# Kernel tuning notes

Hardware: AMD Instinct MI355X
Metric: run time of the kernel (lower is better)

## Reference

```python
import jax, jax.numpy as jnp
import numpy as np

D_MODEL = 512
N_HEAD = 8
D_HEAD = D_MODEL // N_HEAD


def _linear(x, W, b):
    return x @ W + b


def setup_inputs() -> dict:
    key = jax.random.key(0)
    ks = jax.random.split(key, 20)
    B, N, D = 8, 1024, D_MODEL
    H = D // 2
    s = 1.0 / np.sqrt(D)
    s2 = 1.0 / np.sqrt(H)
    inp = {
        'query': jax.random.normal(ks[0], (B, N, D), jnp.float32),
        'key_in': jax.random.normal(ks[1], (B, N, D), jnp.float32),
        'value': jax.random.normal(ks[2], (B, N, D), jnp.float32),
        'Wq': jax.random.normal(ks[3], (D, D), jnp.float32) * s,
        'bq': jnp.zeros((D,), jnp.float32),
        'Wk': jax.random.normal(ks[4], (D, D), jnp.float32) * s,
        'bk': jnp.zeros((D,), jnp.float32),
        'Wv': jax.random.normal(ks[5], (D, D), jnp.float32) * s,
        'bv': jnp.zeros((D,), jnp.float32),
        'Wo': jax.random.normal(ks[6], (D, D), jnp.float32) * s,
        'bo': jnp.zeros((D,), jnp.float32),
        'Ws1': jax.random.normal(ks[7], (D, H), jnp.float32) * s,
        'bs1': jnp.zeros((H,), jnp.float32),
        'Ws2': jax.random.normal(ks[8], (H, D), jnp.float32) * s2,
        'bs2': jnp.zeros((D,), jnp.float32),
        'Wc1': jax.random.normal(ks[9], (D, H), jnp.float32) * s,
        'bc1': jnp.zeros((H,), jnp.float32),
        'Wc2': jax.random.normal(ks[10], (H, D), jnp.float32) * s2,
        'bc2': jnp.zeros((D,), jnp.float32),
    }
    return inp


def reference(query, key_in, value, Wq, bq, Wk, bk, Wv, bv, Wo, bo,
              Ws1, bs1, Ws2, bs2, Wc1, bc1, Wc2, bc2):
    B, N, D = query.shape
    H, Dh = N_HEAD, D_HEAD

    def split_heads(x):  # [b, n, h*d] -> [b, h, n, d]
        return x.reshape(B, N, H, Dh).transpose(0, 2, 1, 3)

    q = split_heads(_linear(query, Wq, bq))
    k = split_heads(_linear(key_in, Wk, bk))
    vv = _linear(value, Wv, bv)  # [b, n, d] == rearrange(v,'b h n d->b n (h d)')

    # spatial gating: Linear-ReLU-Linear-Sigmoid on w_v(value)
    sw = jax.nn.sigmoid(_linear(jax.nn.relu(_linear(vv, Ws1, bs1)), Ws2, bs2))
    v_spatial = split_heads(vv * sw)

    # channel gating: MLP on mean-over-seq profile, broadcast back to seq
    prof = value.mean(axis=1, keepdims=True)  # [b, 1, d]
    cw = jax.nn.sigmoid(_linear(jax.nn.relu(_linear(prof, Wc1, bc1)), Wc2, bc2))
    v_channel = split_heads(_linear(value * cw, Wv, bv))

    v_dual = v_spatial + v_channel

    scores = jnp.einsum('bhqd,bhkd->bhqk', q, k) / np.sqrt(Dh).astype(np.float32)
    attn = jax.nn.softmax(scores, axis=-1)
    out = jnp.einsum('bhqk,bhkd->bhqd', attn, v_dual)
    out = out.transpose(0, 2, 1, 3).reshape(B, N, D)
    return _linear(out, Wo, bo)  # dropout is identity in eval mode
```

## Files before the change

### kernel.cpp

```cpp
#include <hip/hip_runtime.h>

typedef unsigned short u16t;
typedef __bf16  bf8   __attribute__((ext_vector_type(8)));
typedef float   f32x4 __attribute__((ext_vector_type(4)));
typedef unsigned short us4 __attribute__((ext_vector_type(4)));

#define DEV __device__ __forceinline__

DEV float bf2f(u16t u) { union { unsigned u; float f; } x; x.u = ((unsigned)u) << 16; return x.f; }
DEV u16t  f2bf(float f) {
    union { float f; unsigned u; } x; x.f = f;
    unsigned r = x.u + 0x7FFFu + ((x.u >> 16) & 1u);
    return (u16t)(r >> 16);
}
DEV uint4 pack8(const float* v) {
    uint4 r;
    r.x = (unsigned)f2bf(v[0]) | ((unsigned)f2bf(v[1]) << 16);
    r.y = (unsigned)f2bf(v[2]) | ((unsigned)f2bf(v[3]) << 16);
    r.z = (unsigned)f2bf(v[4]) | ((unsigned)f2bf(v[5]) << 16);
    r.w = (unsigned)f2bf(v[6]) | ((unsigned)f2bf(v[7]) << 16);
    return r;
}
DEV void gll16(const void* g, void* l) {
    __builtin_amdgcn_global_load_lds(
        (const __attribute__((address_space(1))) unsigned*)g,
        (__attribute__((address_space(3))) unsigned*)l, 16, 0, 0);
}

#define DMODEL 512
#define SEQ    1024
#define NBATCH 8

__global__ __launch_bounds__(256) void fill_sentinel(float* out, int n)
{
    int i = blockIdx.x * 256 + threadIdx.x;
    if (i < n) out[i] = 100.f;
}

__global__ __launch_bounds__(256) void cvt_value(const float* v, u16t* Vi)
{
    size_t i = ((size_t)blockIdx.x * 256 + threadIdx.x) * 8;
    float4 a = *(const float4*)(v + i), b = *(const float4*)(v + i + 4);
    float o[8] = {a.x, a.y, a.z, a.w, b.x, b.y, b.z, b.w};
    *(uint4*)&Vi[i] = pack8(o);
}

__global__ __launch_bounds__(256) void transpose6(
    const float* s0, const float* s1, const float* s2, const float* s3,
    const float* s4, const float* s5,
    u16t* d0, u16t* d1, u16t* d2, u16t* d3, u16t* d4, u16t* d5)
{
    int z = blockIdx.z;
    const float* S; u16t* D; int R, C;
    switch (z) {
        case 0: S = s0; D = d0; R = 512; C = 512; break;
        case 1: S = s1; D = d1; R = 512; C = 512; break;
        case 2: S = s2; D = d2; R = 512; C = 512; break;
        case 3: S = s3; D = d3; R = 512; C = 512; break;
        case 4: S = s4; D = d4; R = 512; C = 256; break;
        default:S = s5; D = d5; R = 256; C = 512; break;
    }
    int c0 = blockIdx.x * 32, r0 = blockIdx.y * 32;
    if (c0 >= C || r0 >= R) return;
    __shared__ u16t tile[32][33];
    int tx = threadIdx.x & 31, ty = threadIdx.x >> 5;
#pragma unroll
    for (int p = 0; p < 4; ++p) {
        int r = ty + p * 8;
        tile[r][tx] = f2bf(S[(size_t)(r0 + r) * C + c0 + tx]);
    }
    __syncthreads();
#pragma unroll
    for (int p = 0; p < 4; ++p) {
        int r = ty + p * 8;
        D[(size_t)(c0 + r) * R + r0 + tx] = tile[tx][r];
    }
}

__global__ __launch_bounds__(256) void colmean(const u16t* Vi, float* prof)
{
    int b = blockIdx.y, z = blockIdx.z;
    int d = blockIdx.x * 256 + threadIdx.x;
    const u16t* p = Vi + (size_t)b * SEQ * DMODEL + (size_t)z * 64 * DMODEL + d;
    float s = 0.f;
#pragma unroll 8
    for (int n = 0; n < 64; ++n) s += bf2f(p[(size_t)n * DMODEL]);
    atomicAdd(&prof[b * DMODEL + d], s * (1.f / 1024.f));
}

__global__ __launch_bounds__(256) void cmlp(const float* prof,
                                            const float* Wc1, const float* bc1,
                                            const float* Wc2, const float* bc2,
                                            u16t* cw)
{
    int b = blockIdx.x, t = threadIdx.x;
    __shared__ float pf[512];
    __shared__ float hf[256];
    pf[t]       = prof[b * 512 + t];
    pf[t + 256] = prof[b * 512 + t + 256];
    __syncthreads();
    float s = bc1[t];
    for (int k = 0; k < 512; ++k) s += pf[k] * Wc1[(size_t)k * 256 + t];
    hf[t] = fmaxf(s, 0.f);
    __syncthreads();
#pragma unroll
    for (int o = 0; o < 2; ++o) {
        int d = t + o * 256;
        float s2 = bc2[d];
        for (int k = 0; k < 256; ++k) s2 += hf[k] * Wc2[(size_t)k * 512 + d];
        cw[b * 512 + d] = f2bf(1.f / (1.f + __expf(-s2)));
    }
}

__global__ __launch_bounds__(256) void scale_wv(const u16t* WvT, const u16t* cw,
                                                u16t* WvTs)
{
    int b = blockIdx.y;
    int idx = blockIdx.x * 2048 + threadIdx.x * 8;
    int k = idx & 511;
    uint4 wv = *(const uint4*)&WvT[idx];
    uint4 cu = *(const uint4*)&cw[b * 512 + k];
    const u16t* wp = (const u16t*)&wv;
    const u16t* cp = (const u16t*)&cu;
    float o[8];
#pragma unroll
    for (int q = 0; q < 8; ++q) o[q] = bf2f(wp[q]) * bf2f(cp[q]);
    *(uint4*)&WvTs[(size_t)b * 262144 + idx] = pack8(o);
}

template<int NT>
__global__ __launch_bounds__(256) void gemm64(
    const void* A0, const void* A1, const void* A2, const void* A3,
    const u16t* W0, const u16t* W1, const u16t* W2, const u16t* W3,
    const float* B0, const float* B1, const float* B2, const float* B3,
    void* C0, void* C1, void* C2, void* C3,
    int N, int K, int mode,
    const u16t* VVp, u16t* VdTp,
    int araw, int tmask, int outf32, int wbmask)
{
    int z = blockIdx.z;
    const void* A  = (z == 0) ? A0 : (z == 1) ? A1 : (z == 2) ? A2 : A3;
    const u16t* W  = (z == 0) ? W0 : (z == 1) ? W1 : (z == 2) ? W2 : W3;
    const float* Bi = (z == 0) ? B0 : (z == 1) ? B1 : (z == 2) ? B2 : B3;
    void*       C  = (z == 0) ? C0 : (z == 1) ? C1 : (z == 2) ? C2 : C3;

    int af32   = (araw >> z) & 1;
    int tstore = (tmask >> z) & 1;

    int tid = threadIdx.x;
    int w = tid >> 6, lane = tid & 63, quad = lane >> 4, l16 = lane & 15;
    int m0 = blockIdx.x * 64, n0 = blockIdx.y * (NT * 16);
    int bb = m0 >> 10;
    if ((wbmask >> z) & 1) W += (size_t)bb * 262144;

    __shared__ __align__(16) u16t As[64 * 32];
    __shared__ __align__(16) u16t Bs[NT * 16 * 32];

    f32x4 zero = {0.f, 0.f, 0.f, 0.f};
    f32x4 acc[NT];
#pragma unroll
    for (int j = 0; j < NT; ++j) acc[j] = zero;

    for (int k0 = 0; k0 < K; k0 += 32) {
        __syncthreads();
        {
            int r = tid >> 2, g = tid & 3;
            int gs = (g ^ (r & 3)) * 8;
            if (af32) {
                const float* src = (const float*)A + (size_t)(m0 + r) * K + k0 + gs;
                float4 a = *(const float4*)src;
                float4 b = *(const float4*)(src + 4);
                float v[8] = {a.x, a.y, a.z, a.w, b.x, b.y, b.z, b.w};
                *(uint4*)&As[r * 32 + g * 8] = pack8(v);
            } else {
                gll16(&((const u16t*)A)[(size_t)(m0 + r) * K + k0 + gs],
                      &As[(size_t)(w * 64) * 8]);
            }
        }
#pragma unroll
        for (int p = 0; p < NT / 4; ++p) {
            int ci = p * 256 + tid;
            int r = ci >> 2, g = ci & 3;
            int gs = (g ^ (r & 3)) * 8;
            gll16(&W[(size_t)(n0 + r) * K + k0 + gs], &Bs[(size_t)(p * 256 + w * 64) * 8]);
        }
        __syncthreads();
        int sq = (quad ^ (l16 & 3)) * 8;
        bf8 aq = *(const bf8*)&As[(w * 16 + l16) * 32 + sq];
        bf8 bk[NT];
#pragma unroll
        for (int j = 0; j < NT; ++j)
            bk[j] = *(const bf8*)&Bs[(j * 16 + l16) * 32 + sq];
#pragma unroll
        for (int j = 0; j < NT; ++j)
            acc[j] = __builtin_amdgcn_mfma_f32_16x16x32_bf16(aq, bk[j], acc[j], 0, 0, 0);
    }

    int grow0 = m0 + w * 16 + quad * 4;
#pragma unroll
    for (int j = 0; j < NT; ++j) {
        int gcol = n0 + j * 16 + l16;
        float bias = Bi[gcol];
        if (mode == 2) {
            int h = gcol >> 6, dh = gcol & 63;
            int b_ = grow0 >> 10, n_ = grow0 & 1023;
            size_t tbase = (size_t)((b_ * 8 + h) * 64 + dh) * 1024 + n_;
            us4 vc = *(const us4*)&VdTp[tbase];
            us4 pk;
#pragma unroll
            for (int r = 0; r < 4; ++r) {
                float s = acc[j][r] + bias;
                float sw = 1.f / (1.f + __expf(-s));
                float vvv = bf2f(VVp[(size_t)(grow0 + r) * DMODEL + gcol]);
                pk[r] = f2bf(vvv * sw + bf2f(vc[r]));
            }
            *(us4*)&VdTp[tbase] = pk;
        } else if (tstore) {
            int h = gcol >> 6, dh = gcol & 63;
            int b_ = grow0 >> 10, n_ = grow0 & 1023;
            us4 pk;
#pragma unroll
            for (int r = 0; r < 4; ++r) pk[r] = f2bf(acc[j][r] + bias);
            *(us4*)&((u16t*)C)[(size_t)((b_ * 8 + h) * 64 + dh) * 1024 + n_] = pk;
        } else if (outf32) {
#pragma unroll
            for (int r = 0; r < 4; ++r)
                ((float*)C)[(size_t)(grow0 + r) * N + gcol] = acc[j][r] + bias;
        } else {
#pragma unroll
            for (int r = 0; r < 4; ++r) {
                float v = acc[j][r] + bias;
                if (mode == 1) v = fmaxf(v, 0.f);
                ((u16t*)C)[(size_t)(grow0 + r) * N + gcol] = f2bf(v);
            }
        }
    }
}

__global__ __launch_bounds__(256) void attn(const u16t* Q, const u16t* Km,
                                            const u16t* VdT, u16t* Oa)
{
    __shared__ __align__(16) u16t Qs[64 * 64];
    __shared__ __align__(16) u16t Ks[64 * 64];
    __shared__ __align__(16) u16t Vs[64 * 64];
    __shared__ __align__(16) u16t Ps[64 * 64];

    int qt = blockIdx.x, bh = blockIdx.y;
    int b = bh >> 3, h = bh & 7;
    int tid = threadIdx.x;
    int w = tid >> 6, lane = tid & 63, quad = lane >> 4, l16 = lane & 15;
    int l7 = l16 & 7;

    const u16t* Qp = Q   + ((size_t)(b * SEQ + qt * 64)) * DMODEL + h * 64;
    const u16t* Kp = Km  + ((size_t)(b * SEQ)) * DMODEL + h * 64;
    const u16t* Vp = VdT + ((size_t)(b * 8 + h)) * 64 * SEQ;

#pragma unroll
    for (int p = 0; p < 2; ++p) {
        int ci = p * 256 + tid;
        int r = ci >> 3, g = ci & 7;
        int gs = (g ^ (r & 7)) * 8;
        gll16(&Qp[(size_t)r * DMODEL + gs], &Qs[(size_t)(p * 256 + w * 64) * 8]);
    }

    f32x4 zero = {0.f, 0.f, 0.f, 0.f};
    f32x4 oacc[4];
    float l_run[4];
#pragma unroll
    for (int r = 0; r < 4; ++r) { l_run[r] = 0.f; oacc[r] = zero; }

    for (int kt = 0; kt < 16; ++kt) {
        __syncthreads();
#pragma unroll
        for (int p = 0; p < 2; ++p) {
            int ci = p * 256 + tid;
            int r = ci >> 3, g = ci & 7;
            int gs = (g ^ (r & 7)) * 8;
            gll16(&Kp[(size_t)(kt * 64 + r) * DMODEL + gs], &Ks[(size_t)(p * 256 + w * 64) * 8]);
            gll16(&Vp[(size_t)r * SEQ + kt * 64 + gs],      &Vs[(size_t)(p * 256 + w * 64) * 8]);
        }
        __syncthreads();

        f32x4 sacc[4];
#pragma unroll
        for (int j = 0; j < 4; ++j) sacc[j] = zero;
#pragma unroll
        for (int ks = 0; ks < 2; ++ks) {
            int sG = ((ks * 4 + quad) ^ l7) * 8;
            bf8 aq = *(const bf8*)&Qs[(w * 16 + l16) * 64 + sG];
            bf8 bk[4];
#pragma unroll
            for (int j = 0; j < 4; ++j)
                bk[j] = *(const bf8*)&Ks[(j * 16 + l16) * 64 + sG];
#pragma unroll
            for (int j = 0; j < 4; ++j)
                sacc[j] = __builtin_amdgcn_mfma_f32_16x16x32_bf16(aq, bk[j], sacc[j], 0, 0, 0);
        }

#pragma unroll
        for (int r4 = 0; r4 < 4; ++r4) {
            float rsum = 0.f;
            int prow = w * 16 + quad * 4 + r4;
            int pr7 = prow & 7;
#pragma unroll
            for (int j = 0; j < 4; ++j) {
                float p = __expf(fmaf(sacc[j][r4], 0.125f, -4.f));
                rsum += p;
                int G = j * 2 + (l16 >> 3);
                Ps[prow * 64 + ((G ^ pr7) * 8) + l7] = f2bf(p);
            }
#pragma unroll
            for (int d = 1; d < 16; d <<= 1) rsum += __shfl_xor(rsum, d);
            l_run[r4] += rsum;
        }

#pragma unroll
        for (int kk = 0; kk < 2; ++kk) {
            int sG = ((kk * 4 + quad) ^ l7) * 8;
            bf8 ap = *(const bf8*)&Ps[(w * 16 + l16) * 64 + sG];
            bf8 bvf[4];
#pragma unroll
            for (int j = 0; j < 4; ++j)
                bvf[j] = *(const bf8*)&Vs[(j * 16 + l16) * 64 + sG];
#pragma unroll
            for (int j = 0; j < 4; ++j)
                oacc[j] = __builtin_amdgcn_mfma_f32_16x16x32_bf16(ap, bvf[j], oacc[j], 0, 0, 0);
        }
    }

#pragma unroll
    for (int j = 0; j < 4; ++j) {
#pragma unroll
        for (int r4 = 0; r4 < 4; ++r4) {
            int rq = qt * 64 + w * 16 + quad * 4 + r4;
            float v = oacc[j][r4] / l_run[r4];
            Oa[((size_t)(b * SEQ + rq)) * DMODEL + h * 64 + j * 16 + l16] = f2bf(v);
        }
    }
}

extern "C" void kernel_launch(void* const* d_in, const int* in_sizes, int n_in,
                              void* d_out, int out_size, void* d_ws, size_t ws_size,
                              hipStream_t stream)
{
    const float* query  = (const float*)d_in[0];
    const float* key_in = (const float*)d_in[1];
    const float* value  = (const float*)d_in[2];
    const float* Wq  = (const float*)d_in[3];  const float* bq  = (const float*)d_in[4];
    const float* Wk  = (const float*)d_in[5];  const float* bk  = (const float*)d_in[6];
    const float* Wv  = (const float*)d_in[7];  const float* bv  = (const float*)d_in[8];
    const float* Wo  = (const float*)d_in[9];  const float* bo  = (const float*)d_in[10];
    const float* Ws1 = (const float*)d_in[11]; const float* bs1 = (const float*)d_in[12];
    const float* Ws2 = (const float*)d_in[13]; const float* bs2 = (const float*)d_in[14];
    const float* Wc1 = (const float*)d_in[15]; const float* bc1 = (const float*)d_in[16];
    const float* Wc2 = (const float*)d_in[17]; const float* bc2 = (const float*)d_in[18];
    float* out = (float*)d_out;

    u16t* ws = (u16t*)d_ws;
    u16t* WqT  = ws + 0;
    u16t* WkT  = ws + 262144;
    u16t* WvT  = ws + 524288;
    u16t* WoT  = ws + 786432;
    u16t* Ws1T = ws + 1048576;
    u16t* Ws2T = ws + 1179648;
    u16t* WvTs = ws + 1310720;
    u16t* Vi   = ws + 3407872;
    u16t* Qm   = ws + 7602176;
    u16t* Kmm  = ws + 11796480;
    u16t* VV   = ws + 15990784;
    u16t* VdT  = ws + 20185088;
    u16t* cw   = ws + 24379392;
    float* prof = (float*)(ws + 24383488);
    u16t* H1 = Vi;
    u16t* Oa = VV;

    const size_t NEED_BYTES = 24391680ull * 2ull;
    if (ws_size < NEED_BYTES) {
        fill_sentinel<<<(out_size + 255) / 256, 256, 0, stream>>>(out, out_size);
        return;
    }

    hipMemsetAsync((void*)prof, 0, NBATCH * DMODEL * sizeof(float), stream);

    cvt_value<<<2048, 256, 0, stream>>>(value, Vi);
    transpose6<<<dim3(16, 16, 6), 256, 0, stream>>>(Wq, Wk, Wv, Wo, Ws1, Ws2,
                                                    WqT, WkT, WvT, WoT, Ws1T, Ws2T);
    colmean<<<dim3(2, 8, 16), 256, 0, stream>>>(Vi, prof);
    cmlp<<<8, 256, 0, stream>>>(prof, Wc1, bc1, Wc2, bc2, cw);
    scale_wv<<<dim3(128, 8), 256, 0, stream>>>(WvT, cw, WvTs);

    gemm64<8><<<dim3(128, 4, 4), 256, 0, stream>>>(
        query, key_in, Vi, Vi,
        WqT, WkT, WvT, WvTs,
        bq, bk, bv, bv,
        Qm, Kmm, VV, VdT,
        512, 512, 0, nullptr, VdT,
        0x3, 0x8, 0, 0x8);

    gemm64<4><<<dim3(128, 4, 1), 256, 0, stream>>>(
        VV, VV, VV, VV, Ws1T, Ws1T, Ws1T, Ws1T, bs1, bs1, bs1, bs1,
        H1, H1, H1, H1, 256, 512, 1, nullptr, nullptr, 0, 0, 0, 0);

    gemm64<8><<<dim3(128, 4, 1), 256, 0, stream>>>(
        H1, H1, H1, H1, Ws2T, Ws2T, Ws2T, Ws2T, bs2, bs2, bs2, bs2,
        Qm, Qm, Qm, Qm,
        512, 256, 2, VV, VdT, 0, 0, 0, 0);

    attn<<<dim3(16, 64), 256, 0, stream>>>(Qm, Kmm, VdT, Oa);

    gemm64<8><<<dim3(128, 4, 1), 256, 0, stream>>>(
        Oa, Oa, Oa, Oa, WoT, WoT, WoT, WoT, bo, bo, bo, bo,
        out, out, out, out, 512, 512, 0, nullptr, nullptr,
        0, 0, 1, 0);
}
```

Before: 284.3 us.

## Generalize GEMM to 2D warp tiling with per-warp multi-fragment accumulators

Replaces the 64-row, one-warp-per-16-rows GEMM with a templated kernel that arranges the four warps in a 2x2 grid, each computing several 16x16 MFMA tiles in both M and N. A and B fragments loaded from LDS are reused across more MFMAs, which cuts LDS reads per MFMA. The QKV projection moves to 128x128 tiles with half the blocks, and the other GEMMs use 64x128 or 64x64 tiles. A launch-bounds occupancy hint is added. Larger register-held accumulators may lower occupancy, and fewer blocks for the batched projection may underfill the GPU.

```diff
diff --git a/kernel.cpp b/kernel.cpp
--- a/kernel.cpp
+++ b/kernel.cpp
@@ -128,8 +128,8 @@
     *(uint4*)&WvTs[(size_t)b * 262144 + idx] = pack8(o);
 }
 
-template<int NT>
-__global__ __launch_bounds__(256) void gemm64(
+template<int WR, int WC, int WM, int NT>
+__global__ __launch_bounds__(256, 4) void gemmT(
     const void* A0, const void* A1, const void* A2, const void* A3,
     const u16t* W0, const u16t* W1, const u16t* W2, const u16t* W3,
     const float* B0, const float* B1, const float* B2, const float* B3,
@@ -138,6 +138,9 @@
     const u16t* VVp, u16t* VdTp,
     int araw, int tmask, int outf32, int wbmask)
 {
+    constexpr int BM = WR * WM * 16;
+    constexpr int BN = WC * NT * 16;
+
     int z = blockIdx.z;
     const void* A  = (z == 0) ? A0 : (z == 1) ? A1 : (z == 2) ? A2 : A3;
     const u16t* W  = (z == 0) ? W0 : (z == 1) ? W1 : (z == 2) ? W2 : W3;
@@ -149,89 +152,102 @@
 
     int tid = threadIdx.x;
     int w = tid >> 6, lane = tid & 63, quad = lane >> 4, l16 = lane & 15;
-    int m0 = blockIdx.x * 64, n0 = blockIdx.y * (NT * 16);
+    int wr = w / WC, wc = w % WC;
+    int m0 = blockIdx.x * BM, n0 = blockIdx.y * BN;
     int bb = m0 >> 10;
     if ((wbmask >> z) & 1) W += (size_t)bb * 262144;
 
-    __shared__ __align__(16) u16t As[64 * 32];
-    __shared__ __align__(16) u16t Bs[NT * 16 * 32];
+    __shared__ __align__(16) u16t As[BM * 32];
+    __shared__ __align__(16) u16t Bs[BN * 32];
 
     f32x4 zero = {0.f, 0.f, 0.f, 0.f};
-    f32x4 acc[NT];
-#pragma unroll
-    for (int j = 0; j < NT; ++j) acc[j] = zero;
+    f32x4 acc[WM][NT];
+#pragma unroll
+    for (int mi = 0; mi < WM; ++mi)
+#pragma unroll
+        for (int ni = 0; ni < NT; ++ni) acc[mi][ni] = zero;
 
     for (int k0 = 0; k0 < K; k0 += 32) {
         __syncthreads();
-        {
-            int r = tid >> 2, g = tid & 3;
+#pragma unroll
+        for (int p = 0; p < BM / 64; ++p) {
+            int ci = p * 256 + tid;
+            int r = ci >> 2, g = ci & 3;
             int gs = (g ^ (r & 3)) * 8;
             if (af32) {
                 const float* src = (const float*)A + (size_t)(m0 + r) * K + k0 + gs;
                 float4 a = *(const float4*)src;
                 float4 b = *(const float4*)(src + 4);
                 float v[8] = {a.x, a.y, a.z, a.w, b.x, b.y, b.z, b.w};
-                *(uint4*)&As[r * 32 + g * 8] = pack8(v);
+                *(uint4*)&As[(size_t)ci * 8] = pack8(v);
             } else {
                 gll16(&((const u16t*)A)[(size_t)(m0 + r) * K + k0 + gs],
-                      &As[(size_t)(w * 64) * 8]);
+                      &As[(size_t)(p * 256 + w * 64) * 8]);
             }
         }
 #pragma unroll
-        for (int p = 0; p < NT / 4; ++p) {
+        for (int p = 0; p < BN / 64; ++p) {
             int ci = p * 256 + tid;
             int r = ci >> 2, g = ci & 3;
             int gs = (g ^ (r & 3)) * 8;
             gll16(&W[(size_t)(n0 + r) * K + k0 + gs], &Bs[(size_t)(p * 256 + w * 64) * 8]);
         }
         __syncthreads();
-        int sq = (quad ^ (l16 & 3)) * 8;
-        bf8 aq = *(const bf8*)&As[(w * 16 + l16) * 32 + sq];
-        bf8 bk[NT];
-#pragma unroll
-        for (int j = 0; j < NT; ++j)
-            bk[j] = *(const bf8*)&Bs[(j * 16 + l16) * 32 + sq];
-#pragma unroll
-        for (int j = 0; j < NT; ++j)
-            acc[j] = __builtin_amdgcn_mfma_f32_16x16x32_bf16(aq, bk[j], acc[j], 0, 0, 0);
-    }
-
-    int grow0 = m0 + w * 16 + quad * 4;
-#pragma unroll
-    for (int j = 0; j < NT; ++j) {
-        int gcol = n0 + j * 16 + l16;
-        float bias = Bi[gcol];
-        if (mode == 2) {
-            int h = gcol >> 6, dh = gcol & 63;
-            int b_ = grow0 >> 10, n_ = grow0 & 1023;
-            size_t tbase = (size_t)((b_ * 8 + h) * 64 + dh) * 1024 + n_;
-            us4 vc = *(const us4*)&VdTp[tbase];
-            us4 pk;
-#pragma unroll
-            for (int r = 0; r < 4; ++r) {
-                float s = acc[j][r] + bias;
-                float sw = 1.f / (1.f + __expf(-s));
-                float vvv = bf2f(VVp[(size_t)(grow0 + r) * DMODEL + gcol]);
-                pk[r] = f2bf(vvv * sw + bf2f(vc[r]));
-            }
-            *(us4*)&VdTp[tbase] = pk;
-        } else if (tstore) {
-            int h = gcol >> 6, dh = gcol & 63;
-            int b_ = grow0 >> 10, n_ = grow0 & 1023;
-            us4 pk;
-#pragma unroll
-            for (int r = 0; r < 4; ++r) pk[r] = f2bf(acc[j][r] + bias);
-            *(us4*)&((u16t*)C)[(size_t)((b_ * 8 + h) * 64 + dh) * 1024 + n_] = pk;
-        } else if (outf32) {
-#pragma unroll
-            for (int r = 0; r < 4; ++r)
-                ((float*)C)[(size_t)(grow0 + r) * N + gcol] = acc[j][r] + bias;
-        } else {
-#pragma unroll
-            for (int r = 0; r < 4; ++r) {
-                float v = acc[j][r] + bias;
-                if (mode == 1) v = fmaxf(v, 0.f);
-                ((u16t*)C)[(size_t)(grow0 + r) * N + gcol] = f2bf(v);
+
+        int sx = l16 & 3;
+        bf8 af[WM], bfr[NT];
+#pragma unroll
+        for (int mi = 0; mi < WM; ++mi)
+            af[mi] = *(const bf8*)&As[(wr * WM * 16 + mi * 16 + l16) * 32 + ((quad ^ sx) * 8)];
+#pragma unroll
+        for (int ni = 0; ni < NT; ++ni)
+            bfr[ni] = *(const bf8*)&Bs[(wc * NT * 16 + ni * 16 + l16) * 32 + ((quad ^ sx) * 8)];
+#pragma unroll
+        for (int mi = 0; mi < WM; ++mi)
+#pragma unroll
+            for (int ni = 0; ni < NT; ++ni)
+                acc[mi][ni] = __builtin_amdgcn_mfma_f32_16x16x32_bf16(af[mi], bfr[ni], acc[mi][ni], 0, 0, 0);
+    }
+
+#pragma unroll
+    for (int mi = 0; mi < WM; ++mi) {
+        int grow0 = m0 + wr * WM * 16 + mi * 16 + quad * 4;
+#pragma unroll
+        for (int ni = 0; ni < NT; ++ni) {
+            int gcol = n0 + wc * NT * 16 + ni * 16 + l16;
+            float bias = Bi[gcol];
+            if (mode == 2) {
+                int h = gcol >> 6, dh = gcol & 63;
+                int b_ = grow0 >> 10, n_ = grow0 & 1023;
+                size_t tbase = (size_t)((b_ * 8 + h) * 64 + dh) * 1024 + n_;
+                us4 vc = *(const us4*)&VdTp[tbase];
+                us4 pk;
+#pragma unroll
+                for (int r = 0; r < 4; ++r) {
+                    float s = acc[mi][ni][r] + bias;
+                    float sw = 1.f / (1.f + __expf(-s));
+                    float vvv = bf2f(VVp[(size_t)(grow0 + r) * DMODEL + gcol]);
+                    pk[r] = f2bf(vvv * sw + bf2f(vc[r]));
+                }
+                *(us4*)&VdTp[tbase] = pk;
+            } else if (tstore) {
+                int h = gcol >> 6, dh = gcol & 63;
+                int b_ = grow0 >> 10, n_ = grow0 & 1023;
+                us4 pk;
+#pragma unroll
+                for (int r = 0; r < 4; ++r) pk[r] = f2bf(acc[mi][ni][r] + bias);
+                *(us4*)&((u16t*)C)[(size_t)((b_ * 8 + h) * 64 + dh) * 1024 + n_] = pk;
+            } else if (outf32) {
+#pragma unroll
+                for (int r = 0; r < 4; ++r)
+                    ((float*)C)[(size_t)(grow0 + r) * N + gcol] = acc[mi][ni][r] + bias;
+            } else {
+#pragma unroll
+                for (int r = 0; r < 4; ++r) {
+                    float v = acc[mi][ni][r] + bias;
+                    if (mode == 1) v = fmaxf(v, 0.f);
+                    ((u16t*)C)[(size_t)(grow0 + r) * N + gcol] = f2bf(v);
+                }
             }
         }
     }
@@ -389,7 +405,7 @@
     cmlp<<<8, 256, 0, stream>>>(prof, Wc1, bc1, Wc2, bc2, cw);
     scale_wv<<<dim3(128, 8), 256, 0, stream>>>(WvT, cw, WvTs);
 
-    gemm64<8><<<dim3(128, 4, 4), 256, 0, stream>>>(
+    gemmT<2, 2, 4, 4><<<dim3(64, 4, 4), 256, 0, stream>>>(
         query, key_in, Vi, Vi,
         WqT, WkT, WvT, WvTs,
         bq, bk, bv, bv,
@@ -397,18 +413,18 @@
         512, 512, 0, nullptr, VdT,
         0x3, 0x8, 0, 0x8);
 
-    gemm64<4><<<dim3(128, 4, 1), 256, 0, stream>>>(
+    gemmT<2, 2, 2, 2><<<dim3(128, 4, 1), 256, 0, stream>>>(
         VV, VV, VV, VV, Ws1T, Ws1T, Ws1T, Ws1T, bs1, bs1, bs1, bs1,
         H1, H1, H1, H1, 256, 512, 1, nullptr, nullptr, 0, 0, 0, 0);
 
-    gemm64<8><<<dim3(128, 4, 1), 256, 0, stream>>>(
+    gemmT<2, 2, 2, 4><<<dim3(128, 4, 1), 256, 0, stream>>>(
         H1, H1, H1, H1, Ws2T, Ws2T, Ws2T, Ws2T, bs2, bs2, bs2, bs2,
         Qm, Qm, Qm, Qm,
         512, 256, 2, VV, VdT, 0, 0, 0, 0);
 
     attn<<<dim3(16, 64), 256, 0, stream>>>(Qm, Kmm, VdT, Oa);
 
-    gemm64<8><<<dim3(128, 4, 1), 256, 0, stream>>>(
+    gemmT<2, 2, 2, 4><<<dim3(128, 4, 1), 256, 0, stream>>>(
         Oa, Oa, Oa, Oa, WoT, WoT, WoT, WoT, bo, bo, bo, bo,
         out, out, out, out, 512, 512, 0, nullptr, nullptr,
         0, 0, 1, 0);
```

Result: no change. 285.4 us (+0.4%).
